# Kernel tuning notes

Hardware: AMD Instinct MI355X
Metric: run time of the kernel (lower is better)

The kernel has to match this reference:

```python
import jax, jax.numpy as jnp
import numpy as np

NUM_USERS = 100000
NUM_ITEMS = 100000
N_NODES = NUM_USERS + NUM_ITEMS
EMB = 64
N_EDGES = 3200000
N_LAYERS = 3


def setup_inputs() -> dict:
    key = jax.random.key(0)
    k1, k2, k3, k4, k5 = jax.random.split(key, 5)
    user_emb = jax.random.normal(k1, (NUM_USERS, EMB), dtype=jnp.float32)
    item_emb = jax.random.normal(k2, (NUM_ITEMS, EMB), dtype=jnp.float32)
    # COO representation of the normalized adjacency norm_adj (values ~ 1/sqrt(d_i d_j))
    edge_row = jax.random.randint(k3, (N_EDGES,), 0, N_NODES, dtype=jnp.int32)
    edge_col = jax.random.randint(k4, (N_EDGES,), 0, N_NODES, dtype=jnp.int32)
    edge_w = jax.random.uniform(k5, (N_EDGES,), dtype=jnp.float32)
    return {"user_emb": user_emb, "item_emb": item_emb, "edge_w": edge_w,
            "edge_row": edge_row, "edge_col": edge_col}


def _spmm(edge_row, edge_col, edge_w, x):
    # y[r] = sum_{e: row[e]==r} w[e] * x[col[e]]  ==  torch.sparse.mm(norm_adj, x)
    msgs = edge_w[:, None] * x[edge_col]  # [n_edges, E]
    return jax.ops.segment_sum(msgs, edge_row, num_segments=N_NODES)


def reference(user_emb, item_emb, edge_w, edge_row, edge_col):
    ego = jnp.concatenate([user_emb, item_emb], axis=0)  # [N, E]
    acc = jnp.zeros_like(ego)
    for _ in range(N_LAYERS):
        ego = _spmm(edge_row, edge_col, edge_w, ego)
        acc = acc + ego
    final = acc / N_LAYERS  # mean over the n_layers propagated embeddings
    user_all = final[:NUM_USERS]
    item_all = final[NUM_USERS:]
    return (user_all, item_all)
```

## Files before the change

kernel.cpp:

```cpp
#include <hip/hip_runtime.h>
#include <hip/hip_bf16.h>


constexpr int NUM_USERS = 100000;
constexpr int NUM_ITEMS = 100000;
constexpr int N_NODES   = NUM_USERS + NUM_ITEMS;
constexpr int EMB       = 64;
constexpr int N_EDGES   = 3200000;

constexpr int BUCK_SHIFT = 8;
constexpr int NBUCK = (N_NODES + 255) >> BUCK_SHIFT;
constexpr int BIN_BLOCK = 512;
constexpr int EPB = 8192;
constexpr int NBIN_BLOCKS = (N_EDGES + EPB - 1) / EPB;
constexpr int SORT_CAP = 6144;

constexpr int HIST_BLOCKS   = 512;
constexpr int CONCAT_BLOCKS = (N_NODES * 8 + 255) / 256;


__device__ __forceinline__ float bfl(unsigned u) { return __uint_as_float(u << 16); }
__device__ __forceinline__ float bfh(unsigned u) { return __uint_as_float(u & 0xFFFF0000u); }
__device__ __forceinline__ unsigned f2bf(float f) {
    unsigned u = __float_as_uint(f);
    return (u + 0x7FFFu + ((u >> 16) & 1u)) >> 16;
}
__device__ __forceinline__ unsigned pk(float lo, float hi) {
    return f2bf(lo) | (f2bf(hi) << 16);
}


__global__ __launch_bounds__(256) void prep(
    const int* __restrict__ row, int* __restrict__ bcnt,
    const float4* __restrict__ u, const float4* __restrict__ it,
    uint4* __restrict__ ebuf) {
    __shared__ int h[NBUCK];
    if (blockIdx.x < HIST_BLOCKS) {
        for (int i = threadIdx.x; i < NBUCK; i += 256) h[i] = 0;
        __syncthreads();
        int nt = HIST_BLOCKS * 256;
        for (int e = blockIdx.x * 256 + threadIdx.x; e < N_EDGES; e += nt) {
            int r = __builtin_nontemporal_load(&row[e]);
            atomicAdd(&h[r >> BUCK_SHIFT], 1);
        }
        __syncthreads();
        for (int i = threadIdx.x; i < NBUCK; i += 256) {
            int c = h[i];
            if (c) atomicAdd(&bcnt[i], c);
        }
    } else {
        int i = (blockIdx.x - HIST_BLOCKS) * 256 + threadIdx.x;
        if (i >= N_NODES * 8) return;
        const float4* s = (i < NUM_USERS * 8) ? (u + 2 * (size_t)i)
                                              : (it + 2 * ((size_t)i - (size_t)NUM_USERS * 8));
        float4 f0 = s[0], f1 = s[1];
        uint4 o;
        o.x = pk(f0.x, f0.y); o.y = pk(f0.z, f0.w);
        o.z = pk(f1.x, f1.y); o.w = pk(f1.z, f1.w);
        ebuf[i] = o;
    }
}


__global__ __launch_bounds__(1024) void scan_buckets(const int* __restrict__ bcnt,
                                                     int* __restrict__ bbase,
                                                     int* __restrict__ bcursor) {
    __shared__ int lds[1024];
    int t = threadIdx.x;
    int v = (t < NBUCK) ? bcnt[t] : 0;
    lds[t] = v;
    __syncthreads();
    for (int off = 1; off < 1024; off <<= 1) {
        int x = (t >= off) ? lds[t - off] : 0;
        __syncthreads();
        lds[t] += x;
        __syncthreads();
    }
    int excl = lds[t] - v;
    if (t < NBUCK) { bbase[t] = excl; bcursor[t] = excl; }
    if (t == 0) bbase[NBUCK] = N_EDGES;
}

__global__ __launch_bounds__(BIN_BLOCK) void bin_edges(
    const int* __restrict__ row, const int* __restrict__ col,
    const float* __restrict__ w,
    int* __restrict__ bcursor, int2* __restrict__ binned) {
    __shared__ int2 stage[EPB];
    __shared__ int  hcnt[NBUCK];
    __shared__ int  hbase[NBUCK];
    __shared__ int  cursor[NBUCK];
    __shared__ int  lds2[BIN_BLOCK];
    int t = threadIdx.x;
    int e0 = blockIdx.x * EPB;
    int e1 = e0 + EPB; if (e1 > N_EDGES) e1 = N_EDGES;

    for (int i = t; i < NBUCK; i += BIN_BLOCK) hcnt[i] = 0;
    __syncthreads();
    for (int e = e0 + t; e < e1; e += BIN_BLOCK)
        atomicAdd(&hcnt[row[e] >> BUCK_SHIFT], 1);
    __syncthreads();

    for (int i = t; i < NBUCK; i += BIN_BLOCK) {
        int c = hcnt[i];
        hbase[i] = c ? atomicAdd(&bcursor[i], c) : 0;
    }
    int i0 = 2 * t, i1 = 2 * t + 1;
    int c0 = (i0 < NBUCK) ? hcnt[i0] : 0;
    int c1 = (i1 < NBUCK) ? hcnt[i1] : 0;
    lds2[t] = c0 + c1;
    __syncthreads();
    for (int off = 1; off < BIN_BLOCK; off <<= 1) {
        int x = (t >= off) ? lds2[t - off] : 0;
        __syncthreads();
        lds2[t] += x;
        __syncthreads();
    }
    int pairExcl = lds2[t] - (c0 + c1);
    if (i0 < NBUCK) cursor[i0] = pairExcl;
    if (i1 < NBUCK) cursor[i1] = pairExcl + c0;
    __syncthreads();

    for (int e = e0 + t; e < e1; e += BIN_BLOCK) {
        int r  = row[e];
        int bk = r >> BUCK_SHIFT;
        int pos = atomicAdd(&cursor[bk], 1);
        stage[pos] = make_int2(__builtin_nontemporal_load(&col[e]) | ((r & 255) << 18),
                               __float_as_int(__builtin_nontemporal_load(&w[e])));
    }
    __syncthreads();

    int wave = t >> 6;
    int lane = t & 63;
    int sl   = lane & 7;
    constexpr int NWAVE = BIN_BLOCK / 64;
    for (int base = wave * 8; base < NBUCK; base += NWAVE * 8) {
        int bk = base + (lane >> 3);
        if (bk < NBUCK) {
            int c  = hcnt[bk];
            int st = cursor[bk] - c;
            int gp = hbase[bk];
            for (int j = sl; j < c; j += 8)
                binned[gp + j] = stage[st + j];
        }
    }
}

__global__ __launch_bounds__(256) void sort_bucket(
    const int* __restrict__ bbase, const int2* __restrict__ binned,
    int2* __restrict__ sorted, int* __restrict__ row_start) {
    __shared__ int cnt[256];
    __shared__ int sc[256];
    __shared__ int2 buf[SORT_CAP];
    int b = blockIdx.x, t = threadIdx.x;
    int gb = bbase[b];
    int n  = bbase[b + 1] - gb;

    cnt[t] = 0;
    __syncthreads();
    for (int i = t; i < n; i += 256)
        atomicAdd(&cnt[binned[gb + i].x >> 18], 1);
    __syncthreads();

    int v = cnt[t];
    sc[t] = v;
    __syncthreads();
    for (int off = 1; off < 256; off <<= 1) {
        int x = (t >= off) ? sc[t - off] : 0;
        __syncthreads();
        sc[t] += x;
        __syncthreads();
    }
    int excl = sc[t] - v;

    int r = (b << BUCK_SHIFT) + t;
    if (r < N_NODES) row_start[r] = gb + excl;
    if (b == NBUCK - 1 && t == 0) row_start[N_NODES] = N_EDGES;
    __syncthreads();
    cnt[t] = excl;
    __syncthreads();

    for (int i = t; i < n; i += 256) {
        int2 rec = binned[gb + i];
        int rl = rec.x >> 18;
        int k = atomicAdd(&cnt[rl], 1);
        if (k < SORT_CAP)
            buf[k] = make_int2(rec.x & 0x3FFFF, rec.y);
    }
    __syncthreads();
    int m = n < SORT_CAP ? n : SORT_CAP;
    for (int i = t; i < m; i += 256)
        sorted[gb + i] = buf[i];
}


template<bool LAST>
__global__ __launch_bounds__(256) void spmm_bf16(
    const int* __restrict__ row_start, const int2* __restrict__ sorted,
    const uint4* __restrict__ src,
    uint4* __restrict__ y,
    const uint4* __restrict__ y1,
    float4* __restrict__ out)
{
    int r = (blockIdx.x * blockDim.x + threadIdx.x) >> 3;
    int s = threadIdx.x & 7;
    if (r >= N_NODES) return;
    int s0 = row_start[r];
    int s1 = row_start[r + 1];

    float a0 = 0.f, a1 = 0.f, a2 = 0.f, a3 = 0.f;
    float a4 = 0.f, a5 = 0.f, a6 = 0.f, a7 = 0.f;

    for (int base = s0; base < s1; base += 4) {
        int i0 = base;
        int i1 = min(base + 1, N_EDGES - 1);
        int i2 = min(base + 2, N_EDGES - 1);
        int i3 = min(base + 3, N_EDGES - 1);
        int2 e0 = sorted[i0];
        int2 e1 = sorted[i1];
        int2 e2 = sorted[i2];
        int2 e3 = sorted[i3];
        bool v1 = base + 1 < s1, v2 = base + 2 < s1, v3 = base + 3 < s1;
        int   c0 = e0.x;
        int   c1 = v1 ? e1.x : 0;
        int   c2 = v2 ? e2.x : 0;
        int   c3 = v3 ? e3.x : 0;
        float w0 = __int_as_float(e0.y);
        float w1 = v1 ? __int_as_float(e1.y) : 0.f;
        float w2 = v2 ? __int_as_float(e2.y) : 0.f;
        float w3 = v3 ? __int_as_float(e3.y) : 0.f;
        uint4 g0 = src[(size_t)c0 * 8 + s];
        uint4 g1 = src[(size_t)c1 * 8 + s];
        uint4 g2 = src[(size_t)c2 * 8 + s];
        uint4 g3 = src[(size_t)c3 * 8 + s];
#define ACC(vv, wt) \
        a0 = fmaf(wt, bfl(vv.x), a0); a1 = fmaf(wt, bfh(vv.x), a1); \
        a2 = fmaf(wt, bfl(vv.y), a2); a3 = fmaf(wt, bfh(vv.y), a3); \
        a4 = fmaf(wt, bfl(vv.z), a4); a5 = fmaf(wt, bfh(vv.z), a5); \
        a6 = fmaf(wt, bfl(vv.w), a6); a7 = fmaf(wt, bfh(vv.w), a7);
        ACC(g0, w0) ACC(g1, w1) ACC(g2, w2) ACC(g3, w3)
#undef ACC
    }

    if (!LAST) {
        uint4 o;
        o.x = pk(a0, a1); o.y = pk(a2, a3);
        o.z = pk(a4, a5); o.w = pk(a6, a7);
        y[(size_t)r * 8 + s] = o;
    } else {
        uint4 u1 = y1[(size_t)r * 8 + s];
        uint4 u2 = src[(size_t)r * 8 + s];
        constexpr float sc = 1.0f / 3.0f;
        float4 o0, o1;
        o0.x = (a0 + bfl(u1.x) + bfl(u2.x)) * sc;
        o0.y = (a1 + bfh(u1.x) + bfh(u2.x)) * sc;
        o0.z = (a2 + bfl(u1.y) + bfl(u2.y)) * sc;
        o0.w = (a3 + bfh(u1.y) + bfh(u2.y)) * sc;
        o1.x = (a4 + bfl(u1.z) + bfl(u2.z)) * sc;
        o1.y = (a5 + bfh(u1.z) + bfh(u2.z)) * sc;
        o1.z = (a6 + bfl(u1.w) + bfl(u2.w)) * sc;
        o1.w = (a7 + bfh(u1.w) + bfh(u2.w)) * sc;
        size_t ob = (size_t)r * 16 + 2 * s;
        out[ob]     = o0;
        out[ob + 1] = o1;
    }
}


extern "C" void kernel_launch(void* const* d_in, const int* in_sizes, int n_in,
                              void* d_out, int out_size, void* d_ws, size_t ws_size,
                              hipStream_t stream) {
    const float* user_emb = (const float*)d_in[0];
    const float* item_emb = (const float*)d_in[1];
    const float* edge_w   = (const float*)d_in[2];
    const int*   edge_row = (const int*)d_in[3];
    const int*   edge_col = (const int*)d_in[4];

    char* p = (char*)d_ws;
    uint4* ebuf = (uint4*)p;        p += (size_t)N_NODES * 8 * sizeof(uint4);
    uint4* ybuf = (uint4*)p;        p += (size_t)N_NODES * 8 * sizeof(uint4);
    int2*  sorted = (int2*)p;       p += (size_t)N_EDGES * sizeof(int2);
    int*   bcnt = (int*)p;          p += (size_t)NBUCK * sizeof(int);
    int*   bbase = (int*)p;         p += (size_t)(NBUCK + 1) * sizeof(int);
    int*   bcursor = (int*)p;       p += (size_t)NBUCK * sizeof(int);
    int*   row_start = (int*)p;     p += (size_t)(N_NODES + 1) * sizeof(int);
    int2*  binned = (int2*)ybuf;

    hipMemsetAsync(bcnt, 0, (size_t)NBUCK * sizeof(int), stream);

    prep<<<HIST_BLOCKS + CONCAT_BLOCKS, 256, 0, stream>>>(
        edge_row, bcnt, (const float4*)user_emb, (const float4*)item_emb, ebuf);

    scan_buckets<<<1, 1024, 0, stream>>>(bcnt, bbase, bcursor);
    bin_edges<<<NBIN_BLOCKS, BIN_BLOCK, 0, stream>>>(edge_row, edge_col, edge_w,
                                                     bcursor, binned);
    sort_bucket<<<NBUCK, 256, 0, stream>>>(bbase, binned, sorted, row_start);

    int grid = (N_NODES * 8 + 255) / 256;
    spmm_bf16<false><<<grid, 256, 0, stream>>>(row_start, sorted, ebuf, ybuf,
                                               nullptr, nullptr);
    spmm_bf16<false><<<grid, 256, 0, stream>>>(row_start, sorted, ybuf, ebuf,
                                               nullptr, nullptr);
    spmm_bf16<true><<<grid, 256, 0, stream>>>(row_start, sorted, ebuf, nullptr,
                                              ybuf, (float4*)d_out);
}
```

Baseline: 416.1 us.

## Stage per-block edge records in shared memory and unroll gathers by eight

Each SpMM block now handles 32 rows. It cooperatively loads the contiguous range of sorted edge records for those rows into LDS, so the 8 lanes of a row no longer each re-read the same record from global memory. The gather loop is also unrolled to 8 neighbours, giving more outstanding loads per thread. When a block has more edges than the shared buffer holds, it falls back to reading records from global memory. The costs are an added __syncthreads and more register pressure, which may lower occupancy.

```diff
diff --git a/kernel.cpp b/kernel.cpp
--- a/kernel.cpp
+++ b/kernel.cpp
@@ -17,6 +17,9 @@
 
 constexpr int HIST_BLOCKS   = 512;
 constexpr int CONCAT_BLOCKS = (N_NODES * 8 + 255) / 256;
+
+constexpr int ROWS_PER_BLOCK = 32;
+constexpr int ECAP = 1536;
 
 
 __device__ __forceinline__ float bfl(unsigned u) { return __uint_as_float(u << 16); }
@@ -201,45 +204,67 @@
     const uint4* __restrict__ y1,
     float4* __restrict__ out)
 {
-    int r = (blockIdx.x * blockDim.x + threadIdx.x) >> 3;
-    int s = threadIdx.x & 7;
-    if (r >= N_NODES) return;
-    int s0 = row_start[r];
-    int s1 = row_start[r + 1];
+    __shared__ int2 erec[ECAP];
+    __shared__ int  rs[ROWS_PER_BLOCK + 1];
+    int t  = threadIdx.x;
+    int R0 = blockIdx.x * ROWS_PER_BLOCK;
+    if (t <= ROWS_PER_BLOCK) rs[t] = row_start[R0 + t];
+    __syncthreads();
+    int eb0 = rs[0];
+    int n   = rs[ROWS_PER_BLOCK] - eb0;
+
+    int g = t >> 3;
+    int s = t & 7;
+    int r = R0 + g;
+    int s0 = rs[g], s1 = rs[g + 1];
+    int cnt = s1 - s0;
 
     float a0 = 0.f, a1 = 0.f, a2 = 0.f, a3 = 0.f;
     float a4 = 0.f, a5 = 0.f, a6 = 0.f, a7 = 0.f;
 
-    for (int base = s0; base < s1; base += 4) {
-        int i0 = base;
-        int i1 = min(base + 1, N_EDGES - 1);
-        int i2 = min(base + 2, N_EDGES - 1);
-        int i3 = min(base + 3, N_EDGES - 1);
-        int2 e0 = sorted[i0];
-        int2 e1 = sorted[i1];
-        int2 e2 = sorted[i2];
-        int2 e3 = sorted[i3];
-        bool v1 = base + 1 < s1, v2 = base + 2 < s1, v3 = base + 3 < s1;
-        int   c0 = e0.x;
-        int   c1 = v1 ? e1.x : 0;
-        int   c2 = v2 ? e2.x : 0;
-        int   c3 = v3 ? e3.x : 0;
-        float w0 = __int_as_float(e0.y);
-        float w1 = v1 ? __int_as_float(e1.y) : 0.f;
-        float w2 = v2 ? __int_as_float(e2.y) : 0.f;
-        float w3 = v3 ? __int_as_float(e3.y) : 0.f;
-        uint4 g0 = src[(size_t)c0 * 8 + s];
-        uint4 g1 = src[(size_t)c1 * 8 + s];
-        uint4 g2 = src[(size_t)c2 * 8 + s];
-        uint4 g3 = src[(size_t)c3 * 8 + s];
 #define ACC(vv, wt) \
-        a0 = fmaf(wt, bfl(vv.x), a0); a1 = fmaf(wt, bfh(vv.x), a1); \
-        a2 = fmaf(wt, bfl(vv.y), a2); a3 = fmaf(wt, bfh(vv.y), a3); \
-        a4 = fmaf(wt, bfl(vv.z), a4); a5 = fmaf(wt, bfh(vv.z), a5); \
-        a6 = fmaf(wt, bfl(vv.w), a6); a7 = fmaf(wt, bfh(vv.w), a7);
-        ACC(g0, w0) ACC(g1, w1) ACC(g2, w2) ACC(g3, w3)
+    a0 = fmaf(wt, bfl(vv.x), a0); a1 = fmaf(wt, bfh(vv.x), a1); \
+    a2 = fmaf(wt, bfl(vv.y), a2); a3 = fmaf(wt, bfh(vv.y), a3); \
+    a4 = fmaf(wt, bfl(vv.z), a4); a5 = fmaf(wt, bfh(vv.z), a5); \
+    a6 = fmaf(wt, bfl(vv.w), a6); a7 = fmaf(wt, bfh(vv.w), a7);
+
+    if (n <= ECAP) {
+        for (int i = t; i < n; i += 256) erec[i] = sorted[eb0 + i];
+        __syncthreads();
+        int lb = s0 - eb0;
+        for (int k = 0; k < cnt; k += 8) {
+            int   c[8]; float wv[8]; uint4 gr[8];
+#pragma unroll
+            for (int j = 0; j < 8; ++j) {
+                int lk = k + j;
+                bool v = lk < cnt;
+                int2 e = erec[lb + (v ? lk : 0)];
+                c[j]  = v ? e.x : 0;
+                wv[j] = v ? __int_as_float(e.y) : 0.f;
+            }
+#pragma unroll
+            for (int j = 0; j < 8; ++j) gr[j] = src[(size_t)c[j] * 8 + s];
+#pragma unroll
+            for (int j = 0; j < 8; ++j) { ACC(gr[j], wv[j]) }
+        }
+    } else {
+        for (int k = 0; k < cnt; k += 8) {
+            int   c[8]; float wv[8]; uint4 gr[8];
+#pragma unroll
+            for (int j = 0; j < 8; ++j) {
+                int lk = k + j;
+                bool v = lk < cnt;
+                int2 e = sorted[s0 + (v ? lk : 0)];
+                c[j]  = v ? e.x : 0;
+                wv[j] = v ? __int_as_float(e.y) : 0.f;
+            }
+#pragma unroll
+            for (int j = 0; j < 8; ++j) gr[j] = src[(size_t)c[j] * 8 + s];
+#pragma unroll
+            for (int j = 0; j < 8; ++j) { ACC(gr[j], wv[j]) }
+        }
+    }
 #undef ACC
-    }
 
     if (!LAST) {
         uint4 o;
@@ -295,7 +320,7 @@
                                                      bcursor, binned);
     sort_bucket<<<NBUCK, 256, 0, stream>>>(bbase, binned, sorted, row_start);
 
-    int grid = (N_NODES * 8 + 255) / 256;
+    int grid = N_NODES / ROWS_PER_BLOCK;
     spmm_bf16<false><<<grid, 256, 0, stream>>>(row_start, sorted, ebuf, ybuf,
                                                nullptr, nullptr);
     spmm_bf16<false><<<grid, 256, 0, stream>>>(row_start, sorted, ybuf, ebuf,
```

Result: faster. 404.3 us (-2.8%).
